# Kernel optimization log

Measured on AMD Instinct MI355X. Metric: run time of the kernel, lower is better.

Reference implementation:

```python
import jax, jax.numpy as jnp
import numpy as np

N = 4096          # batch of MNIST images
K = 2             # kernel size
NW = K * K        # 4 wires
DIM = 2 ** NW     # 16-dim statevector
NP_ = (28 // K) ** 2  # 196 patches per image


def setup_inputs() -> dict:
    key = jax.random.key(0)
    kx, kw = jax.random.split(key, 2)
    # pixel angles in [0, pi] for the RY encoder
    x = jax.random.uniform(kx, (N, 1, 28, 28), dtype=jnp.float32) * np.float32(np.pi)
    # fixed Haar-random 16x16 unitary standing in for the RandomLayer circuit
    rng = np.random.default_rng(0)
    A = rng.normal(size=(DIM, DIM)) + 1j * rng.normal(size=(DIM, DIM))
    Q, R = np.linalg.qr(A)
    d = np.diagonal(R)
    Q = Q * (d / np.abs(d))  # phase-fix -> Haar unitary
    U_re = jnp.asarray(Q.real, dtype=jnp.float32)
    U_im = jnp.asarray(Q.imag, dtype=jnp.float32)
    # linear head params (kaiming-ish small init)
    W = jax.random.normal(kw, (10, NP_ * NW), dtype=jnp.float32) * 0.02
    b = jnp.zeros((10,), dtype=jnp.float32)
    return {"x": x, "U_re": U_re, "U_im": U_im, "W": W, "b": b}


def reference(x, U_re, U_im, W, b):
    n = x.shape[0]
    # unfold into 2x2 non-overlapping patches, row-major pixels per patch -> [n*196, 4]
    p = x.reshape(n, 14, K, 14, K).transpose(0, 1, 3, 2, 4).reshape(n * NP_, NW)
    half = p * 0.5
    # RY(theta) on |0> -> [cos(theta/2), sin(theta/2)] per wire (real amplitudes)
    v = jnp.stack([jnp.cos(half), jnp.sin(half)], axis=-1)  # [P, 4, 2]
    # product state psi[b0 b1 b2 b3] (wire 0 = most significant bit) -> [P, 16]
    psi = jnp.einsum('pa,pb,pc,pd->pabcd', v[:, 0], v[:, 1], v[:, 2], v[:, 3]).reshape(-1, DIM)
    # random-layer unitary
    U = U_re + 1j * U_im
    phi = psi.astype(U.dtype) @ U.T                        # [P, 16] complex
    probs = jnp.real(phi * jnp.conj(phi))                  # [P, 16]
    # PauliZ expectation per wire: +1 if that bit is 0 else -1
    idx = jnp.arange(DIM)
    shifts = jnp.arange(NW - 1, -1, -1)                    # wire k <-> bit (3-k)
    signs = (1.0 - 2.0 * ((idx[:, None] >> shifts[None, :]) & 1)).astype(probs.dtype)  # [16, 4]
    z = probs @ signs                                      # [P, 4]
    feats = z.reshape(n, NP_ * NW)                         # [n, 784]
    logits = feats @ W.T + b
    return jax.nn.log_softmax(logits, axis=-1)
```

## Files before the change

### kernel.cpp

```cpp
#include <hip/hip_runtime.h>
#include <math.h>

using bf16x8 = __attribute__((ext_vector_type(8))) short;
using f32x16 = __attribute__((ext_vector_type(16))) float;

static __device__ __forceinline__ unsigned cvt_pk_bf16(float lo, float hi) {
    unsigned r;
    asm("v_cvt_pk_bf16_f32 %0, %1, %2" : "=v"(r) : "v"(lo), "v"(hi));
    return r;
}

#define REV_HALF 0.07957747154594767f

__global__ __launch_bounds__(256) void quanv_one(
    const float* __restrict__ x,
    const float* __restrict__ U_re,
    const float* __restrict__ U_im,
    const float* __restrict__ W,
    const float* __restrict__ bias,
    float* __restrict__ out)
{
    __shared__ float4 sfeat4[196];
    __shared__ float  slog[10];

    const int tid  = threadIdx.x;
    const int wv   = tid >> 6;
    const int lane = tid & 63;
    const int l31  = lane & 31;
    const int hi   = lane >> 5;
    const int img  = blockIdx.x;

    const float* Urow = (l31 < 16) ? (U_re + l31 * 16) : (U_im + (l31 - 16) * 16);
    const float4 uf0 = *(const float4*)(Urow + hi * 8);
    const float4 uf1 = *(const float4*)(Urow + hi * 8 + 4);
    union { unsigned u[4]; bf16x8 v; } ua;
    ua.u[0] = cvt_pk_bf16(uf0.x, uf0.y);
    ua.u[1] = cvt_pk_bf16(uf0.z, uf0.w);
    ua.u[2] = cvt_pk_bf16(uf1.x, uf1.y);
    ua.u[3] = cvt_pk_bf16(uf1.z, uf1.w);

    const int p   = (tid < 196) ? tid : 195;
    const int prw = p / 14;
    const int pcl = p - prw * 14;
    const float* xi = x + (size_t)img * 784 + prw * 56 + pcl * 2;
    const float2 t0 = *(const float2*)xi;
    const float2 t1 = *(const float2*)(xi + 28);
    const float r0 = t0.x * REV_HALF, r1 = t0.y * REV_HALF;
    const float r2 = t1.x * REV_HALF, r3 = t1.y * REV_HALF;
    const float s0 = __builtin_amdgcn_sinf(r0), c0 = __builtin_amdgcn_cosf(r0);
    const float s1 = __builtin_amdgcn_sinf(r1), c1 = __builtin_amdgcn_cosf(r1);
    const float s2 = __builtin_amdgcn_sinf(r2), c2 = __builtin_amdgcn_cosf(r2);
    const float s3 = __builtin_amdgcn_sinf(r3), c3 = __builtin_amdgcn_cosf(r3);
    const float a0 = c0 * c1, a1 = c0 * s1, a2 = s0 * c1, a3 = s0 * s1;
    const float b0 = c2 * c3, b1 = c2 * s3, b2 = s2 * c3, b3 = s2 * s3;

    unsigned pL[4], pH[4];
    pL[0] = cvt_pk_bf16(a0 * b0, a0 * b1); pL[1] = cvt_pk_bf16(a0 * b2, a0 * b3);
    pL[2] = cvt_pk_bf16(a1 * b0, a1 * b1); pL[3] = cvt_pk_bf16(a1 * b2, a1 * b3);
    pH[0] = cvt_pk_bf16(a2 * b0, a2 * b1); pH[1] = cvt_pk_bf16(a2 * b2, a2 * b3);
    pH[2] = cvt_pk_bf16(a3 * b0, a3 * b1); pH[3] = cvt_pk_bf16(a3 * b2, a3 * b3);

    f32x16 zacc;
    #pragma unroll
    for (int i = 0; i < 16; ++i) zacc[i] = 0.f;

    #pragma unroll
    for (int T = 0; T < 2; ++T) {
        union { unsigned u[4]; bf16x8 v; } pb;
        #pragma unroll
        for (int c = 0; c < 4; ++c) {
            if (T == 0) {
                const unsigned sw = (unsigned)__shfl_xor((int)pH[c], 32, 64);
                pb.u[c] = hi ? sw : pL[c];
            } else {
                const unsigned sw = (unsigned)__shfl_xor((int)pL[c], 32, 64);
                pb.u[c] = hi ? pH[c] : sw;
            }
        }

        const f32x16 d = __builtin_amdgcn_mfma_f32_32x32x16_bf16(ua.v, pb.v, zacc, 0, 0, 0);

        float P[8];
        #pragma unroll
        for (int r = 0; r < 8; ++r) P[r] = fmaf(d[r], d[r], d[r + 8] * d[r + 8]);

        const float u0 = P[0] + P[1], u1 = P[0] - P[1];
        const float u2 = P[2] + P[3], u3 = P[2] - P[3];
        const float v0 = P[4] + P[5], v1 = P[4] - P[5];
        const float v2 = P[6] + P[7], v3 = P[6] - P[7];
        const float tpp0 = u0 + u2, tb1_0 = u0 - u2, tb0_0 = u1 + u3;
        const float tpp1 = v0 + v2, tb1_1 = v0 - v2, tb0_1 = v1 + v3;
        const float S   = tpp0 + tpp1;
        const float z0p = tpp0 - tpp1;
        const float z2p = tb1_0 + tb1_1;
        const float z3p = tb0_0 + tb0_1;
        const float Sx = __shfl_xor(S, 32, 64);
        const float z0 = z0p + __shfl_xor(z0p, 32, 64);
        const float z2 = z2p + __shfl_xor(z2p, 32, 64);
        const float z3 = z3p + __shfl_xor(z3p, 32, 64);
        const float z1 = hi ? (Sx - S) : (S - Sx);

        if (!hi) {
            const int sp = wv * 64 + T * 32 + l31;
            if (sp < 196) sfeat4[sp] = make_float4(z0, z1, z2, z3);
        }
    }
    __syncthreads();

    const int cs = (wv == 0) ? 0 : (wv == 1) ? 3 : (wv == 2) ? 6 : 8;
    const int nc = (wv <= 1) ? 3 : 2;
    float acc0 = 0.f, acc1 = 0.f, acc2 = 0.f;
    #pragma unroll
    for (int i = 0; i < 4; ++i) {
        const int q = i * 64 + lane;
        if (q < 196) {
            const float4 fv = sfeat4[q];
            const float4 w0 = *(const float4*)(W + (cs + 0) * 784 + q * 4);
            const float4 w1 = *(const float4*)(W + (cs + 1) * 784 + q * 4);
            acc0 = fmaf(w0.x, fv.x, fmaf(w0.y, fv.y, fmaf(w0.z, fv.z, fmaf(w0.w, fv.w, acc0))));
            acc1 = fmaf(w1.x, fv.x, fmaf(w1.y, fv.y, fmaf(w1.z, fv.z, fmaf(w1.w, fv.w, acc1))));
            if (nc > 2) {
                const float4 w2 = *(const float4*)(W + (cs + 2) * 784 + q * 4);
                acc2 = fmaf(w2.x, fv.x, fmaf(w2.y, fv.y, fmaf(w2.z, fv.z, fmaf(w2.w, fv.w, acc2))));
            }
        }
    }
    #pragma unroll
    for (int off = 32; off; off >>= 1) {
        acc0 += __shfl_xor(acc0, off, 64);
        acc1 += __shfl_xor(acc1, off, 64);
        acc2 += __shfl_xor(acc2, off, 64);
    }
    if (lane == 0) {
        slog[cs + 0] = acc0 + bias[cs + 0];
        slog[cs + 1] = acc1 + bias[cs + 1];
        if (nc > 2) slog[cs + 2] = acc2 + bias[cs + 2];
    }
    __syncthreads();

    if (wv == 0 && lane < 16) {
        const float lg = (lane < 10) ? slog[lane] : -1e30f;
        float m = lg;
        #pragma unroll
        for (int off = 8; off; off >>= 1) m = fmaxf(m, __shfl_xor(m, off, 64));
        float e = (lane < 10) ? __expf(lg - m) : 0.f;
        float s = e;
        #pragma unroll
        for (int off = 8; off; off >>= 1) s += __shfl_xor(s, off, 64);
        if (lane < 10) out[(size_t)img * 10 + lane] = lg - m - __logf(s);
    }
}

extern "C" void kernel_launch(void* const* d_in, const int* in_sizes, int n_in,
                              void* d_out, int out_size, void* d_ws, size_t ws_size,
                              hipStream_t stream) {
    const float* x    = (const float*)d_in[0];
    const float* U_re = (const float*)d_in[1];
    const float* U_im = (const float*)d_in[2];
    const float* W    = (const float*)d_in[3];
    const float* bias = (const float*)d_in[4];
    float* out = (float*)d_out;
    const int n = in_sizes[0] / 784;
    quanv_one<<<n, 256, 0, stream>>>(x, U_re, U_im, W, bias, out);
}
```

Before: 17.09 us.

## Process one image per wavefront and fuse linear head without shared memory

Each wavefront now handles a whole image, looping over four patch groups with MFMA, instead of a whole 256-thread block per image. The linear head is accumulated in registers right after each MFMA tile, with lane halves splitting the 10 outputs 5/5. This removes the shared-memory staging and both block barriers, and the log-softmax is computed redundantly per lane. In exchange each wave does more serial work and reads W five rows at a time per tile, so per-wave latency and register pressure go up.

Measured after the change: 17.17 us. Within noise of the previous version (+0.5%).

```diff
diff --git a/kernel.cpp b/kernel.cpp
--- a/kernel.cpp
+++ b/kernel.cpp
@@ -12,23 +12,22 @@
 
 #define REV_HALF 0.07957747154594767f
 
-__global__ __launch_bounds__(256) void quanv_one(
+__global__ __launch_bounds__(256) void quanv_wave(
     const float* __restrict__ x,
     const float* __restrict__ U_re,
     const float* __restrict__ U_im,
     const float* __restrict__ W,
     const float* __restrict__ bias,
-    float* __restrict__ out)
+    float* __restrict__ out,
+    int n_img)
 {
-    __shared__ float4 sfeat4[196];
-    __shared__ float  slog[10];
-
     const int tid  = threadIdx.x;
     const int wv   = tid >> 6;
     const int lane = tid & 63;
     const int l31  = lane & 31;
     const int hi   = lane >> 5;
-    const int img  = blockIdx.x;
+    const int img  = blockIdx.x * 4 + wv;
+    if (img >= n_img) return;
 
     const float* Urow = (l31 < 16) ? (U_re + l31 * 16) : (U_im + (l31 - 16) * 16);
     const float4 uf0 = *(const float4*)(Urow + hi * 8);
@@ -39,116 +38,138 @@
     ua.u[2] = cvt_pk_bf16(uf1.x, uf1.y);
     ua.u[3] = cvt_pk_bf16(uf1.z, uf1.w);
 
-    const int p   = (tid < 196) ? tid : 195;
-    const int prw = p / 14;
-    const int pcl = p - prw * 14;
-    const float* xi = x + (size_t)img * 784 + prw * 56 + pcl * 2;
-    const float2 t0 = *(const float2*)xi;
-    const float2 t1 = *(const float2*)(xi + 28);
-    const float r0 = t0.x * REV_HALF, r1 = t0.y * REV_HALF;
-    const float r2 = t1.x * REV_HALF, r3 = t1.y * REV_HALF;
-    const float s0 = __builtin_amdgcn_sinf(r0), c0 = __builtin_amdgcn_cosf(r0);
-    const float s1 = __builtin_amdgcn_sinf(r1), c1 = __builtin_amdgcn_cosf(r1);
-    const float s2 = __builtin_amdgcn_sinf(r2), c2 = __builtin_amdgcn_cosf(r2);
-    const float s3 = __builtin_amdgcn_sinf(r3), c3 = __builtin_amdgcn_cosf(r3);
-    const float a0 = c0 * c1, a1 = c0 * s1, a2 = s0 * c1, a3 = s0 * s1;
-    const float b0 = c2 * c3, b1 = c2 * s3, b2 = s2 * c3, b3 = s2 * s3;
-
-    unsigned pL[4], pH[4];
-    pL[0] = cvt_pk_bf16(a0 * b0, a0 * b1); pL[1] = cvt_pk_bf16(a0 * b2, a0 * b3);
-    pL[2] = cvt_pk_bf16(a1 * b0, a1 * b1); pL[3] = cvt_pk_bf16(a1 * b2, a1 * b3);
-    pH[0] = cvt_pk_bf16(a2 * b0, a2 * b1); pH[1] = cvt_pk_bf16(a2 * b2, a2 * b3);
-    pH[2] = cvt_pk_bf16(a3 * b0, a3 * b1); pH[3] = cvt_pk_bf16(a3 * b2, a3 * b3);
+    const float* xim = x + (size_t)img * 784;
+    const int cs = hi * 5;
+    float acc0 = 0.f, acc1 = 0.f, acc2 = 0.f, acc3 = 0.f, acc4 = 0.f;
 
     f32x16 zacc;
     #pragma unroll
     for (int i = 0; i < 16; ++i) zacc[i] = 0.f;
 
     #pragma unroll
-    for (int T = 0; T < 2; ++T) {
-        union { unsigned u[4]; bf16x8 v; } pb;
+    for (int r = 0; r < 4; ++r) {
+        const int pown = r * 64 + lane;
+        const int pc   = (pown < 196) ? pown : 195;
+        const int prw  = pc / 14;
+        const int pcl  = pc - prw * 14;
+        const float* xi = xim + prw * 56 + pcl * 2;
+        const float2 t0 = *(const float2*)xi;
+        const float2 t1 = *(const float2*)(xi + 28);
+        const float r0 = t0.x * REV_HALF, r1 = t0.y * REV_HALF;
+        const float r2 = t1.x * REV_HALF, r3 = t1.y * REV_HALF;
+        const float s0 = __builtin_amdgcn_sinf(r0), c0 = __builtin_amdgcn_cosf(r0);
+        const float s1 = __builtin_amdgcn_sinf(r1), c1 = __builtin_amdgcn_cosf(r1);
+        const float s2 = __builtin_amdgcn_sinf(r2), c2 = __builtin_amdgcn_cosf(r2);
+        const float s3 = __builtin_amdgcn_sinf(r3), c3 = __builtin_amdgcn_cosf(r3);
+        const float a0 = c0 * c1, a1 = c0 * s1, a2 = s0 * c1, a3 = s0 * s1;
+        const float b0 = c2 * c3, b1 = c2 * s3, b2 = s2 * c3, b3 = s2 * s3;
+
+        unsigned pL[4], pH[4];
+        pL[0] = cvt_pk_bf16(a0 * b0, a0 * b1); pL[1] = cvt_pk_bf16(a0 * b2, a0 * b3);
+        pL[2] = cvt_pk_bf16(a1 * b0, a1 * b1); pL[3] = cvt_pk_bf16(a1 * b2, a1 * b3);
+        pH[0] = cvt_pk_bf16(a2 * b0, a2 * b1); pH[1] = cvt_pk_bf16(a2 * b2, a2 * b3);
+        pH[2] = cvt_pk_bf16(a3 * b0, a3 * b1); pH[3] = cvt_pk_bf16(a3 * b2, a3 * b3);
+
+        const int ntile = (r < 3) ? 2 : 1;
         #pragma unroll
-        for (int c = 0; c < 4; ++c) {
-            if (T == 0) {
-                const unsigned sw = (unsigned)__shfl_xor((int)pH[c], 32, 64);
-                pb.u[c] = hi ? sw : pL[c];
-            } else {
-                const unsigned sw = (unsigned)__shfl_xor((int)pL[c], 32, 64);
-                pb.u[c] = hi ? pH[c] : sw;
-            }
-        }
+        for (int T = 0; T < 2; ++T) {
+            if (T < ntile) {
+                union { unsigned u[4]; bf16x8 v; } pb;
+                #pragma unroll
+                for (int c = 0; c < 4; ++c) {
+                    if (T == 0) {
+                        const unsigned sw = (unsigned)__shfl_xor((int)pH[c], 32, 64);
+                        pb.u[c] = hi ? sw : pL[c];
+                    } else {
+                        const unsigned sw = (unsigned)__shfl_xor((int)pL[c], 32, 64);
+                        pb.u[c] = hi ? pH[c] : sw;
+                    }
+                }
 
-        const f32x16 d = __builtin_amdgcn_mfma_f32_32x32x16_bf16(ua.v, pb.v, zacc, 0, 0, 0);
+                const f32x16 d = __builtin_amdgcn_mfma_f32_32x32x16_bf16(ua.v, pb.v, zacc, 0, 0, 0);
 
-        float P[8];
-        #pragma unroll
-        for (int r = 0; r < 8; ++r) P[r] = fmaf(d[r], d[r], d[r + 8] * d[r + 8]);
+                float P[8];
+                #pragma unroll
+                for (int q = 0; q < 8; ++q) P[q] = fmaf(d[q], d[q], d[q + 8] * d[q + 8]);
 
-        const float u0 = P[0] + P[1], u1 = P[0] - P[1];
-        const float u2 = P[2] + P[3], u3 = P[2] - P[3];
-        const float v0 = P[4] + P[5], v1 = P[4] - P[5];
-        const float v2 = P[6] + P[7], v3 = P[6] - P[7];
-        const float tpp0 = u0 + u2, tb1_0 = u0 - u2, tb0_0 = u1 + u3;
-        const float tpp1 = v0 + v2, tb1_1 = v0 - v2, tb0_1 = v1 + v3;
-        const float S   = tpp0 + tpp1;
-        const float z0p = tpp0 - tpp1;
-        const float z2p = tb1_0 + tb1_1;
-        const float z3p = tb0_0 + tb0_1;
-        const float Sx = __shfl_xor(S, 32, 64);
-        const float z0 = z0p + __shfl_xor(z0p, 32, 64);
-        const float z2 = z2p + __shfl_xor(z2p, 32, 64);
-        const float z3 = z3p + __shfl_xor(z3p, 32, 64);
-        const float z1 = hi ? (Sx - S) : (S - Sx);
+                const float u0 = P[0] + P[1], u1 = P[0] - P[1];
+                const float u2 = P[2] + P[3], u3 = P[2] - P[3];
+                const float v0 = P[4] + P[5], v1 = P[4] - P[5];
+                const float v2 = P[6] + P[7], v3 = P[6] - P[7];
+                const float tpp0 = u0 + u2, tb1_0 = u0 - u2, tb0_0 = u1 + u3;
+                const float tpp1 = v0 + v2, tb1_1 = v0 - v2, tb0_1 = v1 + v3;
+                const float S   = tpp0 + tpp1;
+                const float z0p = tpp0 - tpp1;
+                const float z2p = tb1_0 + tb1_1;
+                const float z3p = tb0_0 + tb0_1;
+                const float Sx = __shfl_xor(S, 32, 64);
+                float z0 = z0p + __shfl_xor(z0p, 32, 64);
+                float z2 = z2p + __shfl_xor(z2p, 32, 64);
+                float z3 = z3p + __shfl_xor(z3p, 32, 64);
+                float z1 = hi ? (Sx - S) : (S - Sx);
 
-        if (!hi) {
-            const int sp = wv * 64 + T * 32 + l31;
-            if (sp < 196) sfeat4[sp] = make_float4(z0, z1, z2, z3);
-        }
-    }
-    __syncthreads();
-
-    const int cs = (wv == 0) ? 0 : (wv == 1) ? 3 : (wv == 2) ? 6 : 8;
-    const int nc = (wv <= 1) ? 3 : 2;
-    float acc0 = 0.f, acc1 = 0.f, acc2 = 0.f;
-    #pragma unroll
-    for (int i = 0; i < 4; ++i) {
-        const int q = i * 64 + lane;
-        if (q < 196) {
-            const float4 fv = sfeat4[q];
-            const float4 w0 = *(const float4*)(W + (cs + 0) * 784 + q * 4);
-            const float4 w1 = *(const float4*)(W + (cs + 1) * 784 + q * 4);
-            acc0 = fmaf(w0.x, fv.x, fmaf(w0.y, fv.y, fmaf(w0.z, fv.z, fmaf(w0.w, fv.w, acc0))));
-            acc1 = fmaf(w1.x, fv.x, fmaf(w1.y, fv.y, fmaf(w1.z, fv.z, fmaf(w1.w, fv.w, acc1))));
-            if (nc > 2) {
-                const float4 w2 = *(const float4*)(W + (cs + 2) * 784 + q * 4);
-                acc2 = fmaf(w2.x, fv.x, fmaf(w2.y, fv.y, fmaf(w2.z, fv.z, fmaf(w2.w, fv.w, acc2))));
+                int p = r * 64 + T * 32 + l31;
+                if (p >= 196) { z0 = 0.f; z1 = 0.f; z2 = 0.f; z3 = 0.f; p = 195; }
+                const float* wb = W + (size_t)p * 4;
+                const float4 w0 = *(const float4*)(wb + (cs + 0) * 784);
+                const float4 w1 = *(const float4*)(wb + (cs + 1) * 784);
+                const float4 w2 = *(const float4*)(wb + (cs + 2) * 784);
+                const float4 w3 = *(const float4*)(wb + (cs + 3) * 784);
+                const float4 w4 = *(const float4*)(wb + (cs + 4) * 784);
+                acc0 = fmaf(w0.x, z0, fmaf(w0.y, z1, fmaf(w0.z, z2, fmaf(w0.w, z3, acc0))));
+                acc1 = fmaf(w1.x, z0, fmaf(w1.y, z1, fmaf(w1.z, z2, fmaf(w1.w, z3, acc1))));
+                acc2 = fmaf(w2.x, z0, fmaf(w2.y, z1, fmaf(w2.z, z2, fmaf(w2.w, z3, acc2))));
+                acc3 = fmaf(w3.x, z0, fmaf(w3.y, z1, fmaf(w3.z, z2, fmaf(w3.w, z3, acc3))));
+                acc4 = fmaf(w4.x, z0, fmaf(w4.y, z1, fmaf(w4.z, z2, fmaf(w4.w, z3, acc4))));
             }
         }
     }
+
     #pragma unroll
-    for (int off = 32; off; off >>= 1) {
+    for (int off = 16; off; off >>= 1) {
         acc0 += __shfl_xor(acc0, off, 64);
         acc1 += __shfl_xor(acc1, off, 64);
         acc2 += __shfl_xor(acc2, off, 64);
+        acc3 += __shfl_xor(acc3, off, 64);
+        acc4 += __shfl_xor(acc4, off, 64);
     }
-    if (lane == 0) {
-        slog[cs + 0] = acc0 + bias[cs + 0];
-        slog[cs + 1] = acc1 + bias[cs + 1];
-        if (nc > 2) slog[cs + 2] = acc2 + bias[cs + 2];
-    }
-    __syncthreads();
+    const float o0 = __shfl_xor(acc0, 32, 64);
+    const float o1 = __shfl_xor(acc1, 32, 64);
+    const float o2 = __shfl_xor(acc2, 32, 64);
+    const float o3 = __shfl_xor(acc3, 32, 64);
+    const float o4 = __shfl_xor(acc4, 32, 64);
+    const float l0 = (hi ? o0 : acc0) + bias[0];
+    const float l1 = (hi ? o1 : acc1) + bias[1];
+    const float l2 = (hi ? o2 : acc2) + bias[2];
+    const float l3 = (hi ? o3 : acc3) + bias[3];
+    const float l4 = (hi ? o4 : acc4) + bias[4];
+    const float l5 = (hi ? acc0 : o0) + bias[5];
+    const float l6 = (hi ? acc1 : o1) + bias[6];
+    const float l7 = (hi ? acc2 : o2) + bias[7];
+    const float l8 = (hi ? acc3 : o3) + bias[8];
+    const float l9 = (hi ? acc4 : o4) + bias[9];
 
-    if (wv == 0 && lane < 16) {
-        const float lg = (lane < 10) ? slog[lane] : -1e30f;
-        float m = lg;
-        #pragma unroll
-        for (int off = 8; off; off >>= 1) m = fmaxf(m, __shfl_xor(m, off, 64));
-        float e = (lane < 10) ? __expf(lg - m) : 0.f;
-        float s = e;
-        #pragma unroll
-        for (int off = 8; off; off >>= 1) s += __shfl_xor(s, off, 64);
-        if (lane < 10) out[(size_t)img * 10 + lane] = lg - m - __logf(s);
-    }
+    float m = fmaxf(l0, l1);
+    m = fmaxf(m, l2); m = fmaxf(m, l3); m = fmaxf(m, l4);
+    m = fmaxf(m, l5); m = fmaxf(m, l6); m = fmaxf(m, l7);
+    m = fmaxf(m, l8); m = fmaxf(m, l9);
+    const float ssum = __expf(l0 - m) + __expf(l1 - m) + __expf(l2 - m) +
+                       __expf(l3 - m) + __expf(l4 - m) + __expf(l5 - m) +
+                       __expf(l6 - m) + __expf(l7 - m) + __expf(l8 - m) +
+                       __expf(l9 - m);
+    const float lse = m + __logf(ssum);
+
+    float myv = l0;
+    myv = (lane == 1) ? l1 : myv;
+    myv = (lane == 2) ? l2 : myv;
+    myv = (lane == 3) ? l3 : myv;
+    myv = (lane == 4) ? l4 : myv;
+    myv = (lane == 5) ? l5 : myv;
+    myv = (lane == 6) ? l6 : myv;
+    myv = (lane == 7) ? l7 : myv;
+    myv = (lane == 8) ? l8 : myv;
+    myv = (lane == 9) ? l9 : myv;
+    if (lane < 10) out[(size_t)img * 10 + lane] = myv - lse;
 }
 
 extern "C" void kernel_launch(void* const* d_in, const int* in_sizes, int n_in,
@@ -161,5 +182,6 @@
     const float* bias = (const float*)d_in[4];
     float* out = (float*)d_out;
     const int n = in_sizes[0] / 784;
-    quanv_one<<<n, 256, 0, stream>>>(x, U_re, U_im, W, bias, out);
+    const int nblk = (n + 3) / 4;
+    quanv_wave<<<nblk, 256, 0, stream>>>(x, U_re, U_im, W, bias, out, n);
 }
```
